# Optimization experiments

Measured on AMD Instinct MI355X. Metric: run time of the kernel, lower is better.

The kernel has to match this reference:

```python
import jax, jax.numpy as jnp
import numpy as np

B, T, E, H = 8, 1024, 128, 8
S = E // H  # 16, narrow per-head dim


def setup_inputs() -> dict:
    key = jax.random.key(0)
    ks = jax.random.split(key, 7)
    return {
        "x": jax.random.normal(ks[0], (B, T, E), dtype=jnp.float32),
        "masks": jax.random.randint(ks[1], (B, T), 0, 2, dtype=jnp.int32),
        "Wq": jax.random.normal(ks[2], (S, S), dtype=jnp.float32) * 0.05,
        "Wk": jax.random.normal(ks[3], (S, S), dtype=jnp.float32) * 0.05,
        "Wv": jax.random.normal(ks[4], (S, S), dtype=jnp.float32) * 0.05,
        "Wu": jax.random.normal(ks[5], (E, E), dtype=jnp.float32) * 0.05,
        "bu": jnp.zeros((E,), dtype=jnp.float32),
        "temporal_only": 1,
    }


def reference(x, masks, Wq, Wk, Wv, Wu, bu, temporal_only):
    b, t, e = x.shape
    h = H
    s = e // h
    x4 = x.reshape(b, t, h, s)
    # nn.Linear(s, s, bias=False): y = x @ W.T, applied per head
    q = jnp.einsum('bths,ds->bthd', x4, Wq)
    k = jnp.einsum('bths,ds->bthd', x4, Wk)
    v = jnp.einsum('bths,ds->bthd', x4, Wv)
    scale = jnp.float32(e) ** 0.25
    q = q / scale
    k = k / scale
    # (b, h, t, t) attention logits
    dot = jnp.einsum('bqhd,bkhd->bhqk', q, k)
    # temporal_only masking: masks is (b, t), applied on key axis then query axis
    m = masks.astype(bool)
    neg = jnp.float32(-1e9)
    dot = jnp.where(m[:, None, None, :], dot, neg)
    dot = jnp.where(m[:, None, :, None], dot, neg)
    attn = jax.nn.softmax(dot, axis=-1)
    # post-softmax zeroing with the same masks
    attn = jnp.where(m[:, None, None, :], attn, jnp.float32(0.0))
    attn = jnp.where(m[:, None, :, None], attn, jnp.float32(0.0))
    out = jnp.einsum('bhqk,bkhd->bqhd', attn, v).reshape(b, t, h * s)
    return out @ Wu.T + bu
```

## Files before the change

### kernel.cpp

```cpp
#include <hip/hip_runtime.h>

#define NB 8
#define NT 1024
#define NE 128
#define NH 8
#define NS 16

#define WS_Q 0
#define WS_KC 1048576
#define WS_VC 2097152
#define WS_Y 3145728
#define WS_VCNT 4194304

#define WT_PITCH 132

typedef float v2f __attribute__((ext_vector_type(2)));

static __device__ __forceinline__ v2f vlo(const float4 v) { return v2f{v.x, v.y}; }
static __device__ __forceinline__ v2f vhi(const float4 v) { return v2f{v.z, v.w}; }
static __device__ __forceinline__ v2f pfma(v2f a, v2f b, v2f c) {
  return __builtin_elementwise_fma(a, b, c);
}

static __device__ __forceinline__ float fexp2(float x) {
  return __builtin_amdgcn_exp2f(x);
}

static __device__ __forceinline__ void fma4(float4& acc, float s, const float4 v) {
  v2f lo = pfma(v2f{s, s}, vlo(v), vlo(acc));
  v2f hi = pfma(v2f{s, s}, vhi(v), vhi(acc));
  acc.x = lo.x; acc.y = lo.y; acc.z = hi.x; acc.w = hi.y;
}

static __device__ __forceinline__ float dot16p(const float4 q0, const float4 q1,
                                               const float4 q2, const float4 q3,
                                               const float4 k0, const float4 k1,
                                               const float4 k2, const float4 k3) {
  v2f a = vlo(q0) * vlo(k0);
  v2f b = vhi(q0) * vhi(k0);
  a = pfma(vlo(q1), vlo(k1), a);
  b = pfma(vhi(q1), vhi(k1), b);
  a = pfma(vlo(q2), vlo(k2), a);
  b = pfma(vhi(q2), vhi(k2), b);
  a = pfma(vlo(q3), vlo(k3), a);
  b = pfma(vhi(q3), vhi(k3), b);
  v2f c = a + b;
  return c.x + c.y;
}

__global__ __launch_bounds__(256) void qkv_kernel(
    const float* __restrict__ x, const int* __restrict__ masks,
    const float* __restrict__ Wq, const float* __restrict__ Wk,
    const float* __restrict__ Wv, float* __restrict__ Q,
    float* __restrict__ Kc, float* __restrict__ Vc, int* __restrict__ vcount) {
  __shared__ __align__(16) float xs[64 * 20];
  __shared__ int posl[64];
  const int tid = threadIdx.x;
  const int h = blockIdx.x & 7;
  const int rg = blockIdx.x >> 3;
  const int b = rg >> 4;
  const int bt = (rg & 15) << 6;
  {
    const int sr = tid >> 2, sq = tid & 3;
    float4 xv =
        *(const float4*)(x + (size_t)(b * NT + bt + sr) * 128 + h * 16 + sq * 4);
    *(float4*)(xs + sr * 20 + sq * 4) = xv;
  }
  if (tid < 64) {
    int cnt = 0;
    for (int c = 0; c < bt; c += 64)
      cnt += __popcll(__ballot(masks[b * NT + c + tid] != 0));
    int v = masks[b * NT + bt + tid] != 0;
    unsigned long long bal = __ballot(v);
    posl[tid] = v ? (cnt + __popcll(bal & ((1ull << tid) - 1ull))) : -1;
    if (bt == NT - 64 && tid == 0) vcount[b] = cnt + __popcll(bal);
  }
  const int d = tid & 15;
  const int r = (tid >> 4) << 2;
  const float4* wq4 = (const float4*)(Wq + d * 16);
  const float4 wq0 = wq4[0], wq1 = wq4[1], wq2 = wq4[2], wq3 = wq4[3];
  const float4* wk4 = (const float4*)(Wk + d * 16);
  const float4 wk0 = wk4[0], wk1 = wk4[1], wk2 = wk4[2], wk3 = wk4[3];
  const float4* wv4 = (const float4*)(Wv + d * 16);
  const float4 wv0 = wv4[0], wv1 = wv4[1], wv2 = wv4[2], wv3 = wv4[3];
  const float invs = 0.12751744448143132f;
  __syncthreads();
#pragma unroll
  for (int i = 0; i < 4; i++) {
    const int row = r + i;
    const float4* xp = (const float4*)(xs + row * 20);
    const float4 x0 = xp[0], x1 = xp[1], x2 = xp[2], x3 = xp[3];
    float aq = dot16p(x0, x1, x2, x3, wq0, wq1, wq2, wq3);
    float ak = dot16p(x0, x1, x2, x3, wk0, wk1, wk2, wk3);
    float av = dot16p(x0, x1, x2, x3, wv0, wv1, wv2, wv3);
    const int t = bt + row;
    Q[((size_t)(b * NH + h) * NT + t) * NS + d] = aq * invs;
    const int pp = posl[row];
    if (pp >= 0) {
      size_t oc = ((size_t)(b * NH + h) * NT + pp) * NS + d;
      Kc[oc] = ak;
      Vc[oc] = av;
    }
  }
}

__global__ __launch_bounds__(512, 2) void attn_kernel(
    const float* __restrict__ Q, const float* __restrict__ Kc,
    const float* __restrict__ Vc, const int* __restrict__ masks,
    const int* __restrict__ vcount, float* __restrict__ Y) {
  __shared__ __align__(16) float smem[16384];
  float* Ks = smem;
  float* Vs = smem + 8192;
  const int tid = threadIdx.x;
  const int lane = tid & 63;
  const int s = tid >> 6;
  const int bh = blockIdx.x & 63;
  const int qg = blockIdx.x >> 6;
  const int b = bh >> 3, h = bh & 7;
  const int tbase = qg << 8;
  const int nv = vcount[b];

  float4 q[4][4];
#pragma unroll
  for (int qq = 0; qq < 4; qq++) {
    const float4* qg4 =
        (const float4*)(Q + ((size_t)bh * NT + tbase + (qq << 6) + lane) * NS);
    q[qq][0] = qg4[0]; q[qq][1] = qg4[1]; q[qq][2] = qg4[2]; q[qq][3] = qg4[3];
  }
  v2f o[4][8];
  float l[4];
#pragma unroll
  for (int qq = 0; qq < 4; qq++) {
    l[qq] = 0.f;
#pragma unroll
    for (int k = 0; k < 8; k++) o[qq][k] = v2f{0.f, 0.f};
  }

  const int quad = tid & 3;
  const int jr = tid >> 2;

#pragma unroll 1
  for (int k0 = 0; k0 < nv; k0 += 512) {
    const int chunk = (nv - k0 < 512) ? (nv - k0) : 512;
    __syncthreads();
#pragma unroll 1
    for (int p = 0; p < 4; p++) {
      const int row = jr + (p << 7);
      float4 kv = {0, 0, 0, 0};
      if (row < chunk)
        kv = *(const float4*)(Kc + ((size_t)bh * NT + (k0 + row)) * NS +
                              (quad << 2));
      *(float4*)(Ks + row * 16 + (quad << 2)) = kv;
    }
#pragma unroll 1
    for (int p = 0; p < 4; p++) {
      const int row = jr + (p << 7);
      float4 vv = {0, 0, 0, 0};
      if (row < chunk)
        vv = *(const float4*)(Vc + ((size_t)bh * NT + (k0 + row)) * NS +
                              (quad << 2));
      *(float4*)(Vs + row * 16 + (quad << 2)) = vv;
    }
    __syncthreads();
#pragma unroll 2
    for (int g = 0; g < 16; g++) {
      const int rb = s + (g << 5);
      if (rb >= chunk) break;
      float sc[4][4];
#pragma unroll
      for (int i = 0; i < 4; i++) {
        const float4* kr = (const float4*)(Ks + (rb + (i << 3)) * 16);
        const float4 k0v = kr[0], k1v = kr[1], k2v = kr[2], k3v = kr[3];
#pragma unroll
        for (int qq = 0; qq < 4; qq++)
          sc[qq][i] =
              dot16p(q[qq][0], q[qq][1], q[qq][2], q[qq][3], k0v, k1v, k2v, k3v);
      }
#pragma unroll
      for (int i = 0; i < 4; i++)
        if (rb + (i << 3) >= chunk) {
          sc[0][i] = -1e30f; sc[1][i] = -1e30f;
          sc[2][i] = -1e30f; sc[3][i] = -1e30f;
        }
      float p[4][4];
#pragma unroll
      for (int qq = 0; qq < 4; qq++) {
        p[qq][0] = fexp2(sc[qq][0]);
        p[qq][1] = fexp2(sc[qq][1]);
        p[qq][2] = fexp2(sc[qq][2]);
        p[qq][3] = fexp2(sc[qq][3]);
        l[qq] += (p[qq][0] + p[qq][1]) + (p[qq][2] + p[qq][3]);
      }
#pragma unroll
      for (int i = 0; i < 4; i++) {
        const float4* vr = (const float4*)(Vs + (rb + (i << 3)) * 16);
        const float4 v0 = vr[0], v1 = vr[1], v2 = vr[2], v3 = vr[3];
#pragma unroll
        for (int qq = 0; qq < 4; qq++) {
          const v2f pq = {p[qq][i], p[qq][i]};
          o[qq][0] = pfma(pq, vlo(v0), o[qq][0]);
          o[qq][1] = pfma(pq, vhi(v0), o[qq][1]);
          o[qq][2] = pfma(pq, vlo(v1), o[qq][2]);
          o[qq][3] = pfma(pq, vhi(v1), o[qq][3]);
          o[qq][4] = pfma(pq, vlo(v2), o[qq][4]);
          o[qq][5] = pfma(pq, vhi(v2), o[qq][5]);
          o[qq][6] = pfma(pq, vlo(v3), o[qq][6]);
          o[qq][7] = pfma(pq, vhi(v3), o[qq][7]);
        }
      }
    }
  }

  float* om = smem;
#pragma unroll
  for (int ph = 0; ph < 4; ph++) {
    __syncthreads();
    {
      float* pa = om + (s * 64 + lane) * 20;
#pragma unroll
      for (int k = 0; k < 8; k++) *(v2f*)(pa + k * 2) = o[ph][k];
      pa[16] = l[ph];
    }
    __syncthreads();
    {
      const int q8 = tid >> 3;
      const int sub = tid & 7;
      float L = 0.f;
      v2f y = {0.f, 0.f};
#pragma unroll
      for (int ss = 0; ss < 8; ss++) {
        const float* pp = om + (ss * 64 + q8) * 20;
        L += pp[16];
        v2f ov = *(const v2f*)(pp + sub * 2);
        y += ov;
      }
      const int tq = tbase + (ph << 6) + q8;
      const int qm = masks[b * NT + tq];
      const float inv = (qm != 0 && L > 0.f) ? (1.0f / L) : 0.f;
      y *= v2f{inv, inv};
      *(v2f*)(Y + ((size_t)b * NT + tq) * NE + h * NS + sub * 2) = y;
    }
  }
}

__global__ __launch_bounds__(256) void proj_kernel(
    const float* __restrict__ Y, const float* __restrict__ Wu,
    const float* __restrict__ bu, float* __restrict__ out) {
  __shared__ __align__(16) float Wt[64 * WT_PITCH];
  __shared__ __align__(16) float Yt[16 * 128];
  const int tid = threadIdx.x;
  const int r0 = blockIdx.x * 16;
  const float4* yg = (const float4*)(Y + (size_t)r0 * 128);
  float4* yt4 = (float4*)Yt;
  yt4[tid] = yg[tid];
  yt4[tid + 256] = yg[tid + 256];
  const int c0 = (tid & 31) << 2;
  const int rg = (tid >> 5) & 3;
  const int eh = tid >> 7;
  float4 acc0 = {0, 0, 0, 0}, acc1 = {0, 0, 0, 0}, acc2 = {0, 0, 0, 0},
         acc3 = {0, 0, 0, 0};
  for (int e0 = 0; e0 < 128; e0 += 64) {
    __syncthreads();
#pragma unroll
    for (int p = 0; p < 8; p++) {
      int idx = tid + p * 256;
      int c = idx >> 4;
      int es = (idx & 15) << 2;
      float4 w = *(const float4*)(Wu + c * 128 + e0 + es);
      Wt[(es + 0) * WT_PITCH + c] = w.x;
      Wt[(es + 1) * WT_PITCH + c] = w.y;
      Wt[(es + 2) * WT_PITCH + c] = w.z;
      Wt[(es + 3) * WT_PITCH + c] = w.w;
    }
    __syncthreads();
    const int eb = eh << 5;
    const float* y0 = Yt + (rg * 4 + 0) * 128 + e0 + eb;
    const float* y1 = Yt + (rg * 4 + 1) * 128 + e0 + eb;
    const float* y2 = Yt + (rg * 4 + 2) * 128 + e0 + eb;
    const float* y3 = Yt + (rg * 4 + 3) * 128 + e0 + eb;
#pragma unroll 4
    for (int e = 0; e < 32; e += 4) {
      const float* wb = Wt + (eb + e) * WT_PITCH + c0;
      float4 w0 = *(const float4*)(wb + 0 * WT_PITCH);
      float4 w1 = *(const float4*)(wb + 1 * WT_PITCH);
      float4 w2 = *(const float4*)(wb + 2 * WT_PITCH);
      float4 w3 = *(const float4*)(wb + 3 * WT_PITCH);
      float4 ya = *(const float4*)(y0 + e);
      float4 yb = *(const float4*)(y1 + e);
      float4 yc = *(const float4*)(y2 + e);
      float4 yd = *(const float4*)(y3 + e);
      fma4(acc0, ya.x, w0); fma4(acc0, ya.y, w1); fma4(acc0, ya.z, w2); fma4(acc0, ya.w, w3);
      fma4(acc1, yb.x, w0); fma4(acc1, yb.y, w1); fma4(acc1, yb.z, w2); fma4(acc1, yb.w, w3);
      fma4(acc2, yc.x, w0); fma4(acc2, yc.y, w1); fma4(acc2, yc.z, w2); fma4(acc2, yc.w, w3);
      fma4(acc3, yd.x, w0); fma4(acc3, yd.y, w1); fma4(acc3, yd.z, w2); fma4(acc3, yd.w, w3);
    }
  }
  __syncthreads();
  if (eh == 1) {
    float* p = Wt + (tid & 127) * 20;
    *(float4*)(p + 0) = acc0; *(float4*)(p + 4) = acc1;
    *(float4*)(p + 8) = acc2; *(float4*)(p + 12) = acc3;
  }
  __syncthreads();
  if (eh == 0) {
    const float* p = Wt + tid * 20;
    float4 b4 = *(const float4*)(bu + c0);
    float4 q0 = *(const float4*)(p + 0);
    float4 q1 = *(const float4*)(p + 4);
    float4 q2 = *(const float4*)(p + 8);
    float4 q3 = *(const float4*)(p + 12);
    acc0.x += q0.x + b4.x; acc0.y += q0.y + b4.y; acc0.z += q0.z + b4.z; acc0.w += q0.w + b4.w;
    acc1.x += q1.x + b4.x; acc1.y += q1.y + b4.y; acc1.z += q1.z + b4.z; acc1.w += q1.w + b4.w;
    acc2.x += q2.x + b4.x; acc2.y += q2.y + b4.y; acc2.z += q2.z + b4.z; acc2.w += q2.w + b4.w;
    acc3.x += q3.x + b4.x; acc3.y += q3.y + b4.y; acc3.z += q3.z + b4.z; acc3.w += q3.w + b4.w;
    *(float4*)(out + (size_t)(r0 + rg * 4 + 0) * 128 + c0) = acc0;
    *(float4*)(out + (size_t)(r0 + rg * 4 + 1) * 128 + c0) = acc1;
    *(float4*)(out + (size_t)(r0 + rg * 4 + 2) * 128 + c0) = acc2;
    *(float4*)(out + (size_t)(r0 + rg * 4 + 3) * 128 + c0) = acc3;
  }
}

extern "C" void kernel_launch(void* const* d_in, const int* in_sizes, int n_in,
                              void* d_out, int out_size, void* d_ws,
                              size_t ws_size, hipStream_t stream) {
  const float* x = (const float*)d_in[0];
  const int* masks = (const int*)d_in[1];
  const float* Wq = (const float*)d_in[2];
  const float* Wk = (const float*)d_in[3];
  const float* Wv = (const float*)d_in[4];
  const float* Wu = (const float*)d_in[5];
  const float* bu = (const float*)d_in[6];
  float* out = (float*)d_out;

  float* ws = (float*)d_ws;
  float* Q = ws + WS_Q;
  float* Kc = ws + WS_KC;
  float* Vc = ws + WS_VC;
  float* Y = ws + WS_Y;
  int* vcount = (int*)(ws + WS_VCNT);

  qkv_kernel<<<1024, 256, 0, stream>>>(x, masks, Wq, Wk, Wv, Q, Kc, Vc,
                                       vcount);
  attn_kernel<<<4 * NB * NH, 512, 0, stream>>>(Q, Kc, Vc, masks, vcount, Y);
  proj_kernel<<<NB * NT / 16, 256, 0, stream>>>(Y, Wu, bu, out);
}
```

Before: 125.1 us.

## Double attention block size to 1024 threads splitting key rows across 16 waves

Raises the attention kernel to 1024 threads per block, so 16 wavefronts each take a strided subset of the key chunk instead of 8, and each wave does half the inner-loop work. The cross-wave reduction of partial outputs now runs in two passes through the same shared buffer, with extra barriers. The aim is more latency hiding and parallelism with only 256 blocks on the device. The cost is higher register pressure under the new launch bounds and extra synchronisation in the reduction.

```diff
diff --git a/kernel.cpp b/kernel.cpp
--- a/kernel.cpp
+++ b/kernel.cpp
@@ -104,7 +104,7 @@
   }
 }
 
-__global__ __launch_bounds__(512, 2) void attn_kernel(
+__global__ __launch_bounds__(1024, 4) void attn_kernel(
     const float* __restrict__ Q, const float* __restrict__ Kc,
     const float* __restrict__ Vc, const int* __restrict__ masks,
     const int* __restrict__ vcount, float* __restrict__ Y) {
@@ -144,8 +144,8 @@
     const int chunk = (nv - k0 < 512) ? (nv - k0) : 512;
     __syncthreads();
 #pragma unroll 1
-    for (int p = 0; p < 4; p++) {
-      const int row = jr + (p << 7);
+    for (int p = 0; p < 2; p++) {
+      const int row = jr + (p << 8);
       float4 kv = {0, 0, 0, 0};
       if (row < chunk)
         kv = *(const float4*)(Kc + ((size_t)bh * NT + (k0 + row)) * NS +
@@ -153,8 +153,8 @@
       *(float4*)(Ks + row * 16 + (quad << 2)) = kv;
     }
 #pragma unroll 1
-    for (int p = 0; p < 4; p++) {
-      const int row = jr + (p << 7);
+    for (int p = 0; p < 2; p++) {
+      const int row = jr + (p << 8);
       float4 vv = {0, 0, 0, 0};
       if (row < chunk)
         vv = *(const float4*)(Vc + ((size_t)bh * NT + (k0 + row)) * NS +
@@ -163,13 +163,13 @@
     }
     __syncthreads();
 #pragma unroll 2
-    for (int g = 0; g < 16; g++) {
-      const int rb = s + (g << 5);
+    for (int g = 0; g < 8; g++) {
+      const int rb = s + (g << 6);
       if (rb >= chunk) break;
       float sc[4][4];
 #pragma unroll
       for (int i = 0; i < 4; i++) {
-        const float4* kr = (const float4*)(Ks + (rb + (i << 3)) * 16);
+        const float4* kr = (const float4*)(Ks + (rb + (i << 4)) * 16);
         const float4 k0v = kr[0], k1v = kr[1], k2v = kr[2], k3v = kr[3];
 #pragma unroll
         for (int qq = 0; qq < 4; qq++)
@@ -178,7 +178,7 @@
       }
 #pragma unroll
       for (int i = 0; i < 4; i++)
-        if (rb + (i << 3) >= chunk) {
+        if (rb + (i << 4) >= chunk) {
           sc[0][i] = -1e30f; sc[1][i] = -1e30f;
           sc[2][i] = -1e30f; sc[3][i] = -1e30f;
         }
@@ -193,7 +193,7 @@
       }
 #pragma unroll
       for (int i = 0; i < 4; i++) {
-        const float4* vr = (const float4*)(Vs + (rb + (i << 3)) * 16);
+        const float4* vr = (const float4*)(Vs + (rb + (i << 4)) * 16);
         const float4 v0 = vr[0], v1 = vr[1], v2 = vr[2], v3 = vr[3];
 #pragma unroll
         for (int qq = 0; qq < 4; qq++) {
@@ -212,33 +212,48 @@
   }
 
   float* om = smem;
+  const int q8 = tid >> 3;
+  const int sub = tid & 7;
 #pragma unroll
   for (int ph = 0; ph < 4; ph++) {
-    __syncthreads();
-    {
+    v2f ysum = {0.f, 0.f};
+    float Lsum = 0.f;
+    __syncthreads();
+    if (s < 8) {
       float* pa = om + (s * 64 + lane) * 20;
 #pragma unroll
       for (int k = 0; k < 8; k++) *(v2f*)(pa + k * 2) = o[ph][k];
       pa[16] = l[ph];
     }
     __syncthreads();
-    {
-      const int q8 = tid >> 3;
-      const int sub = tid & 7;
-      float L = 0.f;
-      v2f y = {0.f, 0.f};
+    if (tid < 512) {
 #pragma unroll
       for (int ss = 0; ss < 8; ss++) {
         const float* pp = om + (ss * 64 + q8) * 20;
-        L += pp[16];
-        v2f ov = *(const v2f*)(pp + sub * 2);
-        y += ov;
+        Lsum += pp[16];
+        ysum += *(const v2f*)(pp + sub * 2);
+      }
+    }
+    __syncthreads();
+    if (s >= 8) {
+      float* pa = om + ((s - 8) * 64 + lane) * 20;
+#pragma unroll
+      for (int k = 0; k < 8; k++) *(v2f*)(pa + k * 2) = o[ph][k];
+      pa[16] = l[ph];
+    }
+    __syncthreads();
+    if (tid < 512) {
+#pragma unroll
+      for (int ss = 0; ss < 8; ss++) {
+        const float* pp = om + (ss * 64 + q8) * 20;
+        Lsum += pp[16];
+        ysum += *(const v2f*)(pp + sub * 2);
       }
       const int tq = tbase + (ph << 6) + q8;
       const int qm = masks[b * NT + tq];
-      const float inv = (qm != 0 && L > 0.f) ? (1.0f / L) : 0.f;
-      y *= v2f{inv, inv};
-      *(v2f*)(Y + ((size_t)b * NT + tq) * NE + h * NS + sub * 2) = y;
+      const float inv = (qm != 0 && Lsum > 0.f) ? (1.0f / Lsum) : 0.f;
+      ysum *= v2f{inv, inv};
+      *(v2f*)(Y + ((size_t)b * NT + tq) * NE + h * NS + sub * 2) = ysum;
     }
   }
 }
@@ -341,6 +356,6 @@
 
   qkv_kernel<<<1024, 256, 0, stream>>>(x, masks, Wq, Wk, Wv, Q, Kc, Vc,
                                        vcount);
-  attn_kernel<<<4 * NB * NH, 512, 0, stream>>>(Q, Kc, Vc, masks, vcount, Y);
+  attn_kernel<<<4 * NB * NH, 1024, 0, stream>>>(Q, Kc, Vc, masks, vcount, Y);
   proj_kernel<<<NB * NT / 16, 256, 0, stream>>>(Y, Wu, bu, out);
 }
```

Measured after the change: 355.0 us. +183.8%, slower.

## Stage K/V per wave with double-buffered register prefetch, removing block barriers

Applied to the files above, without the earlier changes.

The attention main loop used to stage 512-row K/V chunks cooperatively across the whole block, with two __syncthreads per chunk. Now each wave loads its own 4-key slice: half the lanes fetch K and half fetch V. The slice goes into a private double-buffered LDS region, and the next slice is prefetched into registers while the current one is computed, so no block-wide barrier is needed in the loop. Shared memory shrinks to the size of the final reduction buffer. The cost is that each prefetch only runs one short iteration ahead, so global load latency may be less well hidden than with the old bulk loads.

```diff
diff --git a/kernel.cpp b/kernel.cpp
--- a/kernel.cpp
+++ b/kernel.cpp
@@ -108,9 +108,7 @@
     const float* __restrict__ Q, const float* __restrict__ Kc,
     const float* __restrict__ Vc, const int* __restrict__ masks,
     const int* __restrict__ vcount, float* __restrict__ Y) {
-  __shared__ __align__(16) float smem[16384];
-  float* Ks = smem;
-  float* Vs = smem + 8192;
+  __shared__ __align__(16) float smem[10240];
   const int tid = threadIdx.x;
   const int lane = tid & 63;
   const int s = tid >> 6;
@@ -136,82 +134,85 @@
     for (int k = 0; k < 8; k++) o[qq][k] = v2f{0.f, 0.f};
   }
 
-  const int quad = tid & 3;
-  const int jr = tid >> 2;
-
-#pragma unroll 1
-  for (int k0 = 0; k0 < nv; k0 += 512) {
-    const int chunk = (nv - k0 < 512) ? (nv - k0) : 512;
-    __syncthreads();
-#pragma unroll 1
-    for (int p = 0; p < 4; p++) {
-      const int row = jr + (p << 7);
-      float4 kv = {0, 0, 0, 0};
-      if (row < chunk)
-        kv = *(const float4*)(Kc + ((size_t)bh * NT + (k0 + row)) * NS +
-                              (quad << 2));
-      *(float4*)(Ks + row * 16 + (quad << 2)) = kv;
-    }
-#pragma unroll 1
-    for (int p = 0; p < 4; p++) {
-      const int row = jr + (p << 7);
-      float4 vv = {0, 0, 0, 0};
-      if (row < chunk)
-        vv = *(const float4*)(Vc + ((size_t)bh * NT + (k0 + row)) * NS +
-                              (quad << 2));
-      *(float4*)(Vs + row * 16 + (quad << 2)) = vv;
-    }
-    __syncthreads();
+  const int halfv = lane >> 5;
+  const int r4 = (lane >> 3) & 3;
+  const int pt = lane & 7;
+  const float* __restrict__ srcKV = halfv ? Vc : Kc;
+  float* stg = smem + halfv * 1024 + s * 128;
+  const float* Kr0 = smem + s * 128;
+  const float* Vr0 = smem + 1024 + s * 128;
+  const size_t rowbase = (size_t)bh * NT;
+  const int nu = (nv + 3) >> 2;
+
+  int u = s;
+  v2f rv = {0.f, 0.f};
+  if (u < nu) {
+    const int j = (u << 2) + r4;
+    if (j < nv) rv = *(const v2f*)(srcKV + (rowbase + j) * NS + (pt << 1));
+  }
+  int buf = 0;
 #pragma unroll 2
-    for (int g = 0; g < 16; g++) {
-      const int rb = s + (g << 5);
-      if (rb >= chunk) break;
-      float sc[4][4];
-#pragma unroll
-      for (int i = 0; i < 4; i++) {
-        const float4* kr = (const float4*)(Ks + (rb + (i << 3)) * 16);
-        const float4 k0v = kr[0], k1v = kr[1], k2v = kr[2], k3v = kr[3];
-#pragma unroll
-        for (int qq = 0; qq < 4; qq++)
-          sc[qq][i] =
-              dot16p(q[qq][0], q[qq][1], q[qq][2], q[qq][3], k0v, k1v, k2v, k3v);
+  for (; u < nu; u += 8) {
+    *(v2f*)(stg + (buf << 6) + (r4 << 4) + (pt << 1)) = rv;
+    {
+      const int un = u + 8;
+      rv = v2f{0.f, 0.f};
+      if (un < nu) {
+        const int j = (un << 2) + r4;
+        if (j < nv) rv = *(const v2f*)(srcKV + (rowbase + j) * NS + (pt << 1));
       }
-#pragma unroll
-      for (int i = 0; i < 4; i++)
-        if (rb + (i << 3) >= chunk) {
-          sc[0][i] = -1e30f; sc[1][i] = -1e30f;
-          sc[2][i] = -1e30f; sc[3][i] = -1e30f;
-        }
-      float p[4][4];
+    }
+    const float* Kr = Kr0 + (buf << 6);
+    const float* Vr = Vr0 + (buf << 6);
+    const int j0 = u << 2;
+    float sc[4][4];
+#pragma unroll
+    for (int i = 0; i < 4; i++) {
+      const float4* kr = (const float4*)(Kr + i * 16);
+      const float4 k0v = kr[0], k1v = kr[1], k2v = kr[2], k3v = kr[3];
+#pragma unroll
+      for (int qq = 0; qq < 4; qq++)
+        sc[qq][i] =
+            dot16p(q[qq][0], q[qq][1], q[qq][2], q[qq][3], k0v, k1v, k2v, k3v);
+    }
+#pragma unroll
+    for (int i = 0; i < 4; i++)
+      if (j0 + i >= nv) {
+        sc[0][i] = -1e30f; sc[1][i] = -1e30f;
+        sc[2][i] = -1e30f; sc[3][i] = -1e30f;
+      }
+    float p[4][4];
+#pragma unroll
+    for (int qq = 0; qq < 4; qq++) {
+      p[qq][0] = fexp2(sc[qq][0]);
+      p[qq][1] = fexp2(sc[qq][1]);
+      p[qq][2] = fexp2(sc[qq][2]);
+      p[qq][3] = fexp2(sc[qq][3]);
+      l[qq] += (p[qq][0] + p[qq][1]) + (p[qq][2] + p[qq][3]);
+    }
+#pragma unroll
+    for (int i = 0; i < 4; i++) {
+      const float4* vr = (const float4*)(Vr + i * 16);
+      const float4 v0 = vr[0], v1 = vr[1], v2 = vr[2], v3 = vr[3];
 #pragma unroll
       for (int qq = 0; qq < 4; qq++) {
-        p[qq][0] = fexp2(sc[qq][0]);
-        p[qq][1] = fexp2(sc[qq][1]);
-        p[qq][2] = fexp2(sc[qq][2]);
-        p[qq][3] = fexp2(sc[qq][3]);
-        l[qq] += (p[qq][0] + p[qq][1]) + (p[qq][2] + p[qq][3]);
+        const v2f pq = {p[qq][i], p[qq][i]};
+        o[qq][0] = pfma(pq, vlo(v0), o[qq][0]);
+        o[qq][1] = pfma(pq, vhi(v0), o[qq][1]);
+        o[qq][2] = pfma(pq, vlo(v1), o[qq][2]);
+        o[qq][3] = pfma(pq, vhi(v1), o[qq][3]);
+        o[qq][4] = pfma(pq, vlo(v2), o[qq][4]);
+        o[qq][5] = pfma(pq, vhi(v2), o[qq][5]);
+        o[qq][6] = pfma(pq, vlo(v3), o[qq][6]);
+        o[qq][7] = pfma(pq, vhi(v3), o[qq][7]);
       }
-#pragma unroll
-      for (int i = 0; i < 4; i++) {
-        const float4* vr = (const float4*)(Vs + (rb + (i << 3)) * 16);
-        const float4 v0 = vr[0], v1 = vr[1], v2 = vr[2], v3 = vr[3];
-#pragma unroll
-        for (int qq = 0; qq < 4; qq++) {
-          const v2f pq = {p[qq][i], p[qq][i]};
-          o[qq][0] = pfma(pq, vlo(v0), o[qq][0]);
-          o[qq][1] = pfma(pq, vhi(v0), o[qq][1]);
-          o[qq][2] = pfma(pq, vlo(v1), o[qq][2]);
-          o[qq][3] = pfma(pq, vhi(v1), o[qq][3]);
-          o[qq][4] = pfma(pq, vlo(v2), o[qq][4]);
-          o[qq][5] = pfma(pq, vhi(v2), o[qq][5]);
-          o[qq][6] = pfma(pq, vlo(v3), o[qq][6]);
-          o[qq][7] = pfma(pq, vhi(v3), o[qq][7]);
-        }
-      }
-    }
+    }
+    buf ^= 1;
   }
 
   float* om = smem;
+  const int q8 = tid >> 3;
+  const int sub = tid & 7;
 #pragma unroll
   for (int ph = 0; ph < 4; ph++) {
     __syncthreads();
@@ -223,16 +224,13 @@
     }
     __syncthreads();
     {
-      const int q8 = tid >> 3;
-      const int sub = tid & 7;
       float L = 0.f;
       v2f y = {0.f, 0.f};
 #pragma unroll
       for (int ss = 0; ss < 8; ss++) {
         const float* pp = om + (ss * 64 + q8) * 20;
         L += pp[16];
-        v2f ov = *(const v2f*)(pp + sub * 2);
-        y += ov;
+        y += *(const v2f*)(pp + sub * 2);
       }
       const int tq = tbase + (ph << 6) + q8;
       const int qm = masks[b * NT + tq];
```

After: 144.8 us. 1.16x slower.

## Compact queries to valid positions and skip masked query rows in attention

Applied to the files above, without the earlier changes.

The QKV kernel now writes Q only for unmasked tokens, in the same compacted order as K and V, and records a compacted-to-original index map. The attention kernel splits only the valid queries across its four blocks per head, with a runtime guard that drops unused query slots, and scatters results back through the index map. The projection kernel zeroes the Y rows of masked tokens instead of relying on attention to write zeros. This removes the work spent on roughly half the query rows, which the masks zero out anyway. The cost is runtime branches in the inner loop, which may hurt unrolling or register allocation.

```diff
diff --git a/kernel.cpp b/kernel.cpp
--- a/kernel.cpp
+++ b/kernel.cpp
@@ -10,7 +10,8 @@
 #define WS_KC 1048576
 #define WS_VC 2097152
 #define WS_Y 3145728
-#define WS_VCNT 4194304
+#define WS_VIDX 4194304
+#define WS_VCNT (4194304 + 8192)
 
 #define WT_PITCH 132
 
@@ -52,7 +53,8 @@
     const float* __restrict__ x, const int* __restrict__ masks,
     const float* __restrict__ Wq, const float* __restrict__ Wk,
     const float* __restrict__ Wv, float* __restrict__ Q,
-    float* __restrict__ Kc, float* __restrict__ Vc, int* __restrict__ vcount) {
+    float* __restrict__ Kc, float* __restrict__ Vc, int* __restrict__ vidx,
+    int* __restrict__ vcount) {
   __shared__ __align__(16) float xs[64 * 20];
   __shared__ int posl[64];
   const int tid = threadIdx.x;
@@ -72,7 +74,9 @@
       cnt += __popcll(__ballot(masks[b * NT + c + tid] != 0));
     int v = masks[b * NT + bt + tid] != 0;
     unsigned long long bal = __ballot(v);
-    posl[tid] = v ? (cnt + __popcll(bal & ((1ull << tid) - 1ull))) : -1;
+    int pos = v ? (cnt + __popcll(bal & ((1ull << tid) - 1ull))) : -1;
+    posl[tid] = pos;
+    if (pos >= 0) vidx[b * NT + pos] = bt + tid;
     if (bt == NT - 64 && tid == 0) vcount[b] = cnt + __popcll(bal);
   }
   const int d = tid & 15;
@@ -88,25 +92,23 @@
 #pragma unroll
   for (int i = 0; i < 4; i++) {
     const int row = r + i;
+    const int pp = posl[row];
+    if (pp < 0) continue;
     const float4* xp = (const float4*)(xs + row * 20);
     const float4 x0 = xp[0], x1 = xp[1], x2 = xp[2], x3 = xp[3];
     float aq = dot16p(x0, x1, x2, x3, wq0, wq1, wq2, wq3);
     float ak = dot16p(x0, x1, x2, x3, wk0, wk1, wk2, wk3);
     float av = dot16p(x0, x1, x2, x3, wv0, wv1, wv2, wv3);
-    const int t = bt + row;
-    Q[((size_t)(b * NH + h) * NT + t) * NS + d] = aq * invs;
-    const int pp = posl[row];
-    if (pp >= 0) {
-      size_t oc = ((size_t)(b * NH + h) * NT + pp) * NS + d;
-      Kc[oc] = ak;
-      Vc[oc] = av;
-    }
+    size_t oc = ((size_t)(b * NH + h) * NT + pp) * NS + d;
+    Q[oc] = aq * invs;
+    Kc[oc] = ak;
+    Vc[oc] = av;
   }
 }
 
 __global__ __launch_bounds__(512, 2) void attn_kernel(
     const float* __restrict__ Q, const float* __restrict__ Kc,
-    const float* __restrict__ Vc, const int* __restrict__ masks,
+    const float* __restrict__ Vc, const int* __restrict__ vidx,
     const int* __restrict__ vcount, float* __restrict__ Y) {
   __shared__ __align__(16) float smem[16384];
   float* Ks = smem;
@@ -117,16 +119,26 @@
   const int bh = blockIdx.x & 63;
   const int qg = blockIdx.x >> 6;
   const int b = bh >> 3, h = bh & 7;
-  const int tbase = qg << 8;
   const int nv = vcount[b];
+  const int M = ((nv + 255) >> 8) << 6;
+  const int nq = M >> 6;
+  const int tbase = qg * M;
+  const bool a1 = nq > 1, a2 = nq > 2, a3 = nq > 3;
 
   float4 q[4][4];
-#pragma unroll
-  for (int qq = 0; qq < 4; qq++) {
-    const float4* qg4 =
-        (const float4*)(Q + ((size_t)bh * NT + tbase + (qq << 6) + lane) * NS);
-    q[qq][0] = qg4[0]; q[qq][1] = qg4[1]; q[qq][2] = qg4[2]; q[qq][3] = qg4[3];
-  }
+#define LOADQ(qq)                                                           \
+  {                                                                         \
+    int cq = tbase + ((qq) << 6) + lane;                                    \
+    int cqc = (cq < nv) ? cq : (nv - 1);                                    \
+    const float4* qp = (const float4*)(Q + ((size_t)bh * NT + cqc) * NS);   \
+    q[qq][0] = qp[0]; q[qq][1] = qp[1]; q[qq][2] = qp[2]; q[qq][3] = qp[3]; \
+  }
+  if (nq > 0) LOADQ(0)
+  if (a1) LOADQ(1)
+  if (a2) LOADQ(2)
+  if (a3) LOADQ(3)
+#undef LOADQ
+
   v2f o[4][8];
   float l[4];
 #pragma unroll
@@ -171,10 +183,13 @@
       for (int i = 0; i < 4; i++) {
         const float4* kr = (const float4*)(Ks + (rb + (i << 3)) * 16);
         const float4 k0v = kr[0], k1v = kr[1], k2v = kr[2], k3v = kr[3];
-#pragma unroll
-        for (int qq = 0; qq < 4; qq++)
-          sc[qq][i] =
-              dot16p(q[qq][0], q[qq][1], q[qq][2], q[qq][3], k0v, k1v, k2v, k3v);
+        sc[0][i] = dot16p(q[0][0], q[0][1], q[0][2], q[0][3], k0v, k1v, k2v, k3v);
+        if (a1)
+          sc[1][i] = dot16p(q[1][0], q[1][1], q[1][2], q[1][3], k0v, k1v, k2v, k3v);
+        if (a2)
+          sc[2][i] = dot16p(q[2][0], q[2][1], q[2][2], q[2][3], k0v, k1v, k2v, k3v);
+        if (a3)
+          sc[3][i] = dot16p(q[3][0], q[3][1], q[3][2], q[3][3], k0v, k1v, k2v, k3v);
       }
 #pragma unroll
       for (int i = 0; i < 4; i++)
@@ -183,37 +198,50 @@
           sc[2][i] = -1e30f; sc[3][i] = -1e30f;
         }
       float p[4][4];
-#pragma unroll
-      for (int qq = 0; qq < 4; qq++) {
-        p[qq][0] = fexp2(sc[qq][0]);
-        p[qq][1] = fexp2(sc[qq][1]);
-        p[qq][2] = fexp2(sc[qq][2]);
-        p[qq][3] = fexp2(sc[qq][3]);
-        l[qq] += (p[qq][0] + p[qq][1]) + (p[qq][2] + p[qq][3]);
-      }
+#define SOFTQ(qq)                                          \
+  {                                                        \
+    p[qq][0] = fexp2(sc[qq][0]);                           \
+    p[qq][1] = fexp2(sc[qq][1]);                           \
+    p[qq][2] = fexp2(sc[qq][2]);                           \
+    p[qq][3] = fexp2(sc[qq][3]);                           \
+    l[qq] += (p[qq][0] + p[qq][1]) + (p[qq][2] + p[qq][3]); \
+  }
+      SOFTQ(0)
+      if (a1) SOFTQ(1)
+      if (a2) SOFTQ(2)
+      if (a3) SOFTQ(3)
+#undef SOFTQ
 #pragma unroll
       for (int i = 0; i < 4; i++) {
         const float4* vr = (const float4*)(Vs + (rb + (i << 3)) * 16);
         const float4 v0 = vr[0], v1 = vr[1], v2 = vr[2], v3 = vr[3];
-#pragma unroll
-        for (int qq = 0; qq < 4; qq++) {
-          const v2f pq = {p[qq][i], p[qq][i]};
-          o[qq][0] = pfma(pq, vlo(v0), o[qq][0]);
-          o[qq][1] = pfma(pq, vhi(v0), o[qq][1]);
-          o[qq][2] = pfma(pq, vlo(v1), o[qq][2]);
-          o[qq][3] = pfma(pq, vhi(v1), o[qq][3]);
-          o[qq][4] = pfma(pq, vlo(v2), o[qq][4]);
-          o[qq][5] = pfma(pq, vhi(v2), o[qq][5]);
-          o[qq][6] = pfma(pq, vlo(v3), o[qq][6]);
-          o[qq][7] = pfma(pq, vhi(v3), o[qq][7]);
-        }
+#define PVQ(qq)                                      \
+  {                                                  \
+    const v2f pq = {p[qq][i], p[qq][i]};             \
+    o[qq][0] = pfma(pq, vlo(v0), o[qq][0]);          \
+    o[qq][1] = pfma(pq, vhi(v0), o[qq][1]);          \
+    o[qq][2] = pfma(pq, vlo(v1), o[qq][2]);          \
+    o[qq][3] = pfma(pq, vhi(v1), o[qq][3]);          \
+    o[qq][4] = pfma(pq, vlo(v2), o[qq][4]);          \
+    o[qq][5] = pfma(pq, vhi(v2), o[qq][5]);          \
+    o[qq][6] = pfma(pq, vlo(v3), o[qq][6]);          \
+    o[qq][7] = pfma(pq, vhi(v3), o[qq][7]);          \
+  }
+        PVQ(0)
+        if (a1) PVQ(1)
+        if (a2) PVQ(2)
+        if (a3) PVQ(3)
+#undef PVQ
       }
     }
   }
 
   float* om = smem;
+  const int q8 = tid >> 3;
+  const int sub = tid & 7;
 #pragma unroll
   for (int ph = 0; ph < 4; ph++) {
+    if (ph >= nq) break;
     __syncthreads();
     {
       float* pa = om + (s * 64 + lane) * 20;
@@ -223,37 +251,44 @@
     }
     __syncthreads();
     {
-      const int q8 = tid >> 3;
-      const int sub = tid & 7;
-      float L = 0.f;
-      v2f y = {0.f, 0.f};
-#pragma unroll
-      for (int ss = 0; ss < 8; ss++) {
-        const float* pp = om + (ss * 64 + q8) * 20;
-        L += pp[16];
-        v2f ov = *(const v2f*)(pp + sub * 2);
-        y += ov;
+      const int cq = tbase + (ph << 6) + q8;
+      if (cq < nv) {
+        float L = 0.f;
+        v2f y = {0.f, 0.f};
+#pragma unroll
+        for (int ss = 0; ss < 8; ss++) {
+          const float* pp = om + (ss * 64 + q8) * 20;
+          L += pp[16];
+          y += *(const v2f*)(pp + sub * 2);
+        }
+        const int tq = vidx[b * NT + cq];
+        const float inv = (L > 0.f) ? (1.0f / L) : 0.f;
+        y *= v2f{inv, inv};
+        *(v2f*)(Y + ((size_t)b * NT + tq) * NE + h * NS + sub * 2) = y;
       }
-      const int tq = tbase + (ph << 6) + q8;
-      const int qm = masks[b * NT + tq];
-      const float inv = (qm != 0 && L > 0.f) ? (1.0f / L) : 0.f;
-      y *= v2f{inv, inv};
-      *(v2f*)(Y + ((size_t)b * NT + tq) * NE + h * NS + sub * 2) = y;
     }
   }
 }
 
 __global__ __launch_bounds__(256) void proj_kernel(
-    const float* __restrict__ Y, const float* __restrict__ Wu,
-    const float* __restrict__ bu, float* __restrict__ out) {
+    const float* __restrict__ Y, const int* __restrict__ masks,
+    const float* __restrict__ Wu, const float* __restrict__ bu,
+    float* __restrict__ out) {
   __shared__ __align__(16) float Wt[64 * WT_PITCH];
   __shared__ __align__(16) float Yt[16 * 128];
   const int tid = threadIdx.x;
   const int r0 = blockIdx.x * 16;
   const float4* yg = (const float4*)(Y + (size_t)r0 * 128);
   float4* yt4 = (float4*)Yt;
-  yt4[tid] = yg[tid];
-  yt4[tid + 256] = yg[tid + 256];
+  {
+    const float4 z = {0, 0, 0, 0};
+    const int m0 = masks[r0 + (tid >> 5)];
+    const int m1 = masks[r0 + 8 + (tid >> 5)];
+    float4 v0 = yg[tid];
+    float4 v1 = yg[tid + 256];
+    yt4[tid] = m0 ? v0 : z;
+    yt4[tid + 256] = m1 ? v1 : z;
+  }
   const int c0 = (tid & 31) << 2;
   const int rg = (tid >> 5) & 3;
   const int eh = tid >> 7;
@@ -337,10 +372,11 @@
   float* Kc = ws + WS_KC;
   float* Vc = ws + WS_VC;
   float* Y = ws + WS_Y;
+  int* vidx = (int*)(ws + WS_VIDX);
   int* vcount = (int*)(ws + WS_VCNT);
 
-  qkv_kernel<<<1024, 256, 0, stream>>>(x, masks, Wq, Wk, Wv, Q, Kc, Vc,
+  qkv_kernel<<<1024, 256, 0, stream>>>(x, masks, Wq, Wk, Wv, Q, Kc, Vc, vidx,
                                        vcount);
-  attn_kernel<<<4 * NB * NH, 512, 0, stream>>>(Q, Kc, Vc, masks, vcount, Y);
-  proj_kernel<<<NB * NT / 16, 256, 0, stream>>>(Y, Wu, bu, out);
-}
+  attn_kernel<<<4 * NB * NH, 512, 0, stream>>>(Q, Kc, Vc, vidx, vcount, Y);
+  proj_kernel<<<NB * NT / 16, 256, 0, stream>>>(Y, masks, Wu, bu, out);
+}
```

New measurement: 216.6 us. 73.1% more time.
